# Performance work log

Hardware: AMD Instinct MI355X
Metric: run time of the kernel (lower is better)

Reference implementation:

```python
import jax, jax.numpy as jnp
import numpy as np

B, LQ, LIM = 4, 640, 1296
D_MODEL, NHEAD, DFF, MAX_DIST = 768, 12, 3072, 100
DK = D_MODEL // NHEAD
EPS = 1e-5


def _layer_norm(x, g, b):
    mu = jnp.mean(x, axis=-1, keepdims=True)
    var = jnp.mean(jnp.square(x - mu), axis=-1, keepdims=True)
    return (x - mu) * jax.lax.rsqrt(var + EPS) * g + b


def setup_inputs() -> dict:
    key = jax.random.key(0)
    ks = jax.random.split(key, 24)
    s = 0.02
    inp = {
        "docqa": jax.random.normal(ks[0], (B, LQ, D_MODEL), jnp.float32),
        "im_tokens": jax.random.normal(ks[1], (B, LIM, D_MODEL), jnp.float32),
        "docqa_x": jax.random.randint(ks[2], (B, LQ), 0, 1000, jnp.int32),
        "docqa_y": jax.random.randint(ks[3], (B, LQ), 0, 1000, jnp.int32),
        "im_tokens_x": jax.random.randint(ks[4], (B, LIM), 0, 1000, jnp.int32),
        "im_tokens_y": jax.random.randint(ks[5], (B, LIM), 0, 1000, jnp.int32),
        # attention projection params
        "Wq": jax.random.normal(ks[6], (D_MODEL, D_MODEL), jnp.float32) * s,
        "bq": jnp.zeros((D_MODEL,), jnp.float32),
        "Wk": jax.random.normal(ks[7], (D_MODEL, D_MODEL), jnp.float32) * s,
        "bk": jnp.zeros((D_MODEL,), jnp.float32),
        "Wv": jax.random.normal(ks[8], (D_MODEL, D_MODEL), jnp.float32) * s,
        "bv": jnp.zeros((D_MODEL,), jnp.float32),
        "Wo": jax.random.normal(ks[9], (D_MODEL, D_MODEL), jnp.float32) * s,
        "bo": jnp.zeros((D_MODEL,), jnp.float32),
        # relative position bias tables: (2*max_dist+1, nhead) per axis
        "bias_x": jax.random.normal(ks[10], (2 * MAX_DIST + 1, NHEAD), jnp.float32) * s,
        "bias_y": jax.random.normal(ks[11], (2 * MAX_DIST + 1, NHEAD), jnp.float32) * s,
        # FFN
        "W1": jax.random.normal(ks[12], (D_MODEL, DFF), jnp.float32) * s,
        "b1": jnp.zeros((DFF,), jnp.float32),
        "W2": jax.random.normal(ks[13], (DFF, D_MODEL), jnp.float32) * s,
        "b2": jnp.zeros((D_MODEL,), jnp.float32),
        # LayerNorms
        "g1": jnp.ones((D_MODEL,), jnp.float32),
        "be1": jnp.zeros((D_MODEL,), jnp.float32),
        "g2": jnp.ones((D_MODEL,), jnp.float32),
        "be2": jnp.zeros((D_MODEL,), jnp.float32),
    }
    return inp


def reference(docqa, im_tokens, docqa_x, docqa_y, im_tokens_x, im_tokens_y,
              Wq, bq, Wk, bk, Wv, bv, Wo, bo, bias_x, bias_y,
              W1, b1, W2, b2, g1, be1, g2, be2):
    # keys/values attend over concatenated image tokens + docqa tokens
    full = jnp.concatenate([im_tokens, docqa], axis=1)            # (B, Lk, D)
    full_x = jnp.concatenate([im_tokens_x, docqa_x], axis=1)      # (B, Lk)
    full_y = jnp.concatenate([im_tokens_y, docqa_y], axis=1)

    q = (docqa @ Wq + bq).reshape(B, LQ, NHEAD, DK)               # (B,Lq,H,Dk)
    k = (full @ Wk + bk).reshape(B, LQ + LIM, NHEAD, DK)
    v = (full @ Wv + bv).reshape(B, LQ + LIM, NHEAD, DK)

    scores = jnp.einsum("bqhd,bkhd->bhqk", q, k) / jnp.sqrt(jnp.float32(DK))

    # relative-position bias, clamped to [-max_dist, max_dist]
    rel_x = jnp.clip(docqa_x[:, :, None] - full_x[:, None, :], -MAX_DIST, MAX_DIST) + MAX_DIST
    rel_y = jnp.clip(docqa_y[:, :, None] - full_y[:, None, :], -MAX_DIST, MAX_DIST) + MAX_DIST
    pos_bias = bias_x[rel_x] + bias_y[rel_y]                      # (B,Lq,Lk,H)
    scores = scores + jnp.transpose(pos_bias, (0, 3, 1, 2))       # (B,H,Lq,Lk)

    attn = jax.nn.softmax(scores, axis=-1)
    ctx = jnp.einsum("bhqk,bkhd->bqhd", attn, v).reshape(B, LQ, D_MODEL)
    attn_out = ctx @ Wo + bo

    # residual + norm + FFN + residual + norm (dropout=0 in eval)
    src = _layer_norm(docqa + attn_out, g1, be1)
    ffn = jnp.maximum(src @ W1 + b1, 0.0) @ W2 + b2
    src = _layer_norm(src + ffn, g2, be2)
    return src
```

## Files before the change

### kernel.cpp

```cpp
#include <hip/hip_runtime.h>
#include <hip/hip_bf16.h>

constexpr int B      = 4;
constexpr int LQ     = 640;
constexpr int LIM    = 1296;
constexpr int LK     = LQ + LIM;
constexpr int DM     = 768;
constexpr int NHEAD  = 12;
constexpr int DK     = 64;
constexpr int DFF    = 3072;
constexpr int MAXD   = 100;
constexpr int M_DOC  = B * LQ;
constexpr int M_FULL = B * LK;
constexpr size_t ML_CNT = (size_t)B * NHEAD * LQ;
constexpr int NPREP  = M_FULL * (DM / 8) / 256;
constexpr int NSPLIT = 3;

typedef __attribute__((ext_vector_type(8))) short bf16x8_t;
typedef __attribute__((ext_vector_type(4))) float f32x4_t;

__device__ __forceinline__ float b2f(__hip_bfloat16 x) { return __bfloat162float(x); }

__device__ __forceinline__ float ldf(const void* p, size_t i, int f32flag) {
    return f32flag ? ((const float*)p)[i]
                   : b2f(((const __hip_bfloat16*)p)[i]);
}

__device__ __forceinline__ void gl_lds16(const void* g, void* l) {
    __builtin_amdgcn_global_load_lds(
        (const __attribute__((address_space(1))) unsigned int*)g,
        (__attribute__((address_space(3))) unsigned int*)l, 16, 0, 0);
}

__device__ __forceinline__ void wtrans_tile(const void* W, __hip_bfloat16* Wt,
                                            int f32, int K, int N, int n0, int k0,
                                            __hip_bfloat16 (*t)[33])
{
    const int tx = threadIdx.x & 31, ty = threadIdx.x >> 5;
#pragma unroll
    for (int j = 0; j < 4; ++j) {
        int k = ty + j * 8;
        t[k][tx] = __float2bfloat16(ldf(W, (size_t)(k0 + k) * N + n0 + tx, f32));
    }
    __syncthreads();
#pragma unroll
    for (int j = 0; j < 4; ++j) {
        int n = ty + j * 8;
        Wt[(size_t)(n0 + n) * K + k0 + tx] = t[tx][n];
    }
}

__global__ __launch_bounds__(256)
void prep_wt3_kernel(const void* __restrict__ g1, int* __restrict__ flagp,
                     const void* __restrict__ im, const void* __restrict__ docqa,
                     const int* __restrict__ dqx, const int* __restrict__ dqy,
                     const int* __restrict__ imx, const int* __restrict__ imy,
                     const void* __restrict__ Wq, const void* __restrict__ Wk,
                     const void* __restrict__ Wv,
                     __hip_bfloat16* __restrict__ fullA,
                     int* __restrict__ cxy,
                     __hip_bfloat16* __restrict__ Wt3)
{
    __shared__ __hip_bfloat16 t[32][33];
    const bool f32 = ((*(const unsigned*)g1) & 0xFFFFu) == 0u;
    const int bx = blockIdx.x;

    if (bx >= NPREP) {
        const int id  = bx - NPREP;
        const int wid = id / 576;
        const int tt  = id % 576;
        const void* W = (wid == 0) ? Wq : (wid == 1) ? Wk : Wv;
        wtrans_tile(W, Wt3 + (size_t)wid * DM * DM, f32 ? 1 : 0, DM, DM,
                    (tt % 24) * 32, (tt / 24) * 32, t);
        return;
    }

    if (bx == 0 && threadIdx.x == 0) *flagp = f32 ? 1 : 0;

    const int gid = bx * 256 + threadIdx.x;
    if (gid < B * LK) {
        int b = gid / LK, l = gid - b * LK;
        const int x = (l < LIM) ? imx[b * LIM + l] : dqx[b * LQ + l - LIM];
        const int y = (l < LIM) ? imy[b * LIM + l] : dqy[b * LQ + l - LIM];
        cxy[gid] = (x & 0xFFFF) | (y << 16);
    }

    const int row = gid / (DM / 8);
    const int col = (gid - row * (DM / 8)) * 8;
    const int b   = row / LK;
    const int l   = row - b * LK;
    const size_t srow = (l < LIM) ? ((size_t)(b * LIM + l)) * DM
                                  : ((size_t)(b * LQ + (l - LIM))) * DM;
    const void* src = (l < LIM) ? im : docqa;
    union { bf16x8_t v; __hip_bfloat16 h[8]; } pk;
    if (f32) {
        const float4* fp = (const float4*)((const float*)src + srow + col);
        float4 a = fp[0], c = fp[1];
        pk.h[0] = __float2bfloat16(a.x); pk.h[1] = __float2bfloat16(a.y);
        pk.h[2] = __float2bfloat16(a.z); pk.h[3] = __float2bfloat16(a.w);
        pk.h[4] = __float2bfloat16(c.x); pk.h[5] = __float2bfloat16(c.y);
        pk.h[6] = __float2bfloat16(c.z); pk.h[7] = __float2bfloat16(c.w);
    } else {
        pk.v = *(const bf16x8_t*)((const __hip_bfloat16*)src + srow + col);
    }
    *(bf16x8_t*)(fullA + (size_t)row * DM + col) = pk.v;
}

__global__ __launch_bounds__(256)
void qkv_gemm(const __hip_bfloat16* __restrict__ fullA,
              const __hip_bfloat16* __restrict__ Wt3,
              const void* __restrict__ bq,
              const void* __restrict__ bk,
              const void* __restrict__ bv,
              __hip_bfloat16* __restrict__ qout,
              __hip_bfloat16* __restrict__ kb,
              __hip_bfloat16* __restrict__ vtb,
              const int* __restrict__ flagp)
{
    __shared__ __hip_bfloat16 Als[128 * 32];
    __shared__ __hip_bfloat16 Bls[128 * 32];

    const int f32  = *flagp;
    const int tid  = threadIdx.x;
    const int lane = tid & 63;
    const int wave = tid >> 6;
    const int quad = lane >> 4;
    const int c16  = lane & 15;

    const int id = blockIdx.x;
    int n0, m0;
    if (id < 732) {
        n0 = DM + (id % 12) * 128;
        m0 = (id / 12) * 128;
    } else {
        const int t = id - 732;
        n0 = (t % 6) * 128;
        m0 = (t / 6) * 128;
    }
    const int seg = n0 / DM;

    const int wm   = (wave >> 1) * 64;
    const int wn   = (wave & 1) * 64;
    constexpr int K = DM;

    f32x4_t acc[4][4] = {};

    for (int k0 = 0; k0 < K; k0 += 32) {
#pragma unroll
        for (int p = 0; p < 2; ++p) {
            const int lin = p * 64 + lane;
            int row = wave * 32 + (lin >> 2);
            int gr  = m0 + row;
            if (seg == 0) {
                const int bb = gr / LQ;
                gr = bb * LK + LIM + (gr - bb * LQ);
            } else if (gr > M_FULL - 1) gr = M_FULL - 1;
            gl_lds16(fullA + (size_t)gr * K + k0 + (lin & 3) * 8,
                     Als + wave * 1024 + p * 512);
        }
#pragma unroll
        for (int p = 0; p < 2; ++p) {
            const int lin = p * 64 + lane;
            const int row = wave * 32 + (lin >> 2);
            gl_lds16(Wt3 + (size_t)(n0 + row) * K + k0 + (lin & 3) * 8,
                     Bls + wave * 1024 + p * 512);
        }
        __syncthreads();

        bf16x8_t af[4], bfr[4];
#pragma unroll
        for (int i = 0; i < 4; ++i)
            af[i] = *(const bf16x8_t*)(Als + (wm + i * 16 + c16) * 32 + quad * 8);
#pragma unroll
        for (int j = 0; j < 4; ++j)
            bfr[j] = *(const bf16x8_t*)(Bls + (wn + j * 16 + c16) * 32 + quad * 8);
#pragma unroll
        for (int i = 0; i < 4; ++i)
#pragma unroll
            for (int j = 0; j < 4; ++j)
                acc[i][j] = __builtin_amdgcn_mfma_f32_16x16x32_bf16(af[i], bfr[j], acc[i][j], 0, 0, 0);
        __syncthreads();
    }

    const void* bptr = (seg == 0) ? bq : (seg == 1) ? bk : bv;
#pragma unroll
    for (int j = 0; j < 4; ++j) {
        const int col  = n0 + wn + j * 16 + c16;
        const int ncol = col - seg * DM;
        const float bj = ldf(bptr, ncol, f32);
        if (seg == 2) {
            const int h = ncol >> 6, d = ncol & 63;
#pragma unroll
            for (int i = 0; i < 4; ++i) {
                const int rowb = m0 + wm + i * 16 + quad * 4;
                const int bb0  = rowb / LK;
                const int l0   = rowb - bb0 * LK;
                if (l0 + 3 < LK && rowb + 3 < M_FULL) {
                    union { ushort4 u4; __hip_bfloat16 hh[4]; } pk;
#pragma unroll
                    for (int r = 0; r < 4; ++r)
                        pk.hh[r] = __float2bfloat16(acc[i][j][r] + bj);
                    *(ushort4*)(vtb + ((size_t)((bb0 * NHEAD + h) * DK + d)) * LK + l0) = pk.u4;
                } else {
#pragma unroll
                    for (int r = 0; r < 4; ++r) {
                        const int row = rowb + r;
                        if (row < M_FULL) {
                            int bb = row / LK, l = row - bb * LK;
                            vtb[((size_t)((bb * NHEAD + h) * DK + d)) * LK + l] =
                                __float2bfloat16(acc[i][j][r] + bj);
                        }
                    }
                }
            }
        } else if (seg == 1) {
#pragma unroll
            for (int i = 0; i < 4; ++i) {
                const int rowb = m0 + wm + i * 16 + quad * 4;
#pragma unroll
                for (int r = 0; r < 4; ++r) {
                    const int row = rowb + r;
                    if (row < M_FULL)
                        kb[(size_t)row * DM + ncol] = __float2bfloat16(acc[i][j][r] + bj);
                }
            }
        } else {
#pragma unroll
            for (int i = 0; i < 4; ++i) {
                const int rowb = m0 + wm + i * 16 + quad * 4;
#pragma unroll
                for (int r = 0; r < 4; ++r)
                    qout[(size_t)(rowb + r) * DM + ncol] =
                        __float2bfloat16((acc[i][j][r] + bj) * 0.125f);
            }
        }
    }
}

__global__ __launch_bounds__(256)
void mfma_gemm_relu(const __hip_bfloat16* __restrict__ Abf,
                    const __hip_bfloat16* __restrict__ Wt,
                    const void* __restrict__ bias,
                    __hip_bfloat16* __restrict__ Cc,
                    const int* __restrict__ flagp,
                    int M, int N, int K)
{
    __shared__ __hip_bfloat16 Als[128 * 32];
    __shared__ __hip_bfloat16 Bls[128 * 32];

    const int f32  = *flagp;
    const int tid  = threadIdx.x;
    const int lane = tid & 63;
    const int wave = tid >> 6;
    const int quad = lane >> 4;
    const int c16  = lane & 15;
    const int n0   = blockIdx.x * 128;
    const int m0   = blockIdx.y * 128;
    const int wm   = (wave >> 1) * 64;
    const int wn   = (wave & 1) * 64;

    f32x4_t acc[4][4] = {};

    for (int k0 = 0; k0 < K; k0 += 32) {
#pragma unroll
        for (int p = 0; p < 2; ++p) {
            const int lin = p * 64 + lane;
            int row = wave * 32 + (lin >> 2);
            int gr  = m0 + row; if (gr > M - 1) gr = M - 1;
            gl_lds16(Abf + (size_t)gr * K + k0 + (lin & 3) * 8, Als + wave * 1024 + p * 512);
        }
#pragma unroll
        for (int p = 0; p < 2; ++p) {
            const int lin = p * 64 + lane;
            const int row = wave * 32 + (lin >> 2);
            gl_lds16(Wt + (size_t)(n0 + row) * K + k0 + (lin & 3) * 8,
                     Bls + wave * 1024 + p * 512);
        }
        __syncthreads();

        bf16x8_t af[4], bfr[4];
#pragma unroll
        for (int i = 0; i < 4; ++i)
            af[i] = *(const bf16x8_t*)(Als + (wm + i * 16 + c16) * 32 + quad * 8);
#pragma unroll
        for (int j = 0; j < 4; ++j)
            bfr[j] = *(const bf16x8_t*)(Bls + (wn + j * 16 + c16) * 32 + quad * 8);
#pragma unroll
        for (int i = 0; i < 4; ++i)
#pragma unroll
            for (int j = 0; j < 4; ++j)
                acc[i][j] = __builtin_amdgcn_mfma_f32_16x16x32_bf16(af[i], bfr[j], acc[i][j], 0, 0, 0);
        __syncthreads();
    }

#pragma unroll
    for (int j = 0; j < 4; ++j) {
        const int col = n0 + wn + j * 16 + c16;
        const float bj = ldf(bias, col, f32);
#pragma unroll
        for (int i = 0; i < 4; ++i) {
            const int rowb = m0 + wm + i * 16 + quad * 4;
#pragma unroll
            for (int r = 0; r < 4; ++r) {
                const int row = rowb + r;
                if (row < M) {
                    float v = fmaxf(acc[i][j][r] + bj, 0.f);
                    Cc[(size_t)row * N + col] = __float2bfloat16(v);
                }
            }
        }
    }
}

__global__ __launch_bounds__(256)
void sk_gemm(const __hip_bfloat16* __restrict__ Abf,
             const __hip_bfloat16* __restrict__ Wt,
             float* __restrict__ Cc,
             int M, int N, int K, int S)
{
    __shared__ __hip_bfloat16 Als[128 * 32];
    __shared__ __hip_bfloat16 Bls[128 * 32];

    const int tid  = threadIdx.x;
    const int lane = tid & 63;
    const int wave = tid >> 6;
    const int quad = lane >> 4;
    const int c16  = lane & 15;
    const int n0   = blockIdx.x * 128;
    const int m0   = blockIdx.y * 128;
    const int wm   = (wave >> 1) * 64;
    const int wn   = (wave & 1) * 64;
    const int kchunk = K / S;
    const int kbeg = blockIdx.z * kchunk;

    f32x4_t acc[4][4] = {};

    for (int k0 = kbeg; k0 < kbeg + kchunk; k0 += 32) {
#pragma unroll
        for (int p = 0; p < 2; ++p) {
            const int lin = p * 64 + lane;
            int row = wave * 32 + (lin >> 2);
            int gr  = m0 + row; if (gr > M - 1) gr = M - 1;
            gl_lds16(Abf + (size_t)gr * K + k0 + (lin & 3) * 8, Als + wave * 1024 + p * 512);
        }
#pragma unroll
        for (int p = 0; p < 2; ++p) {
            const int lin = p * 64 + lane;
            const int row = wave * 32 + (lin >> 2);
            gl_lds16(Wt + (size_t)(n0 + row) * K + k0 + (lin & 3) * 8,
                     Bls + wave * 1024 + p * 512);
        }
        __syncthreads();

        bf16x8_t af[4], bfr[4];
#pragma unroll
        for (int i = 0; i < 4; ++i)
            af[i] = *(const bf16x8_t*)(Als + (wm + i * 16 + c16) * 32 + quad * 8);
#pragma unroll
        for (int j = 0; j < 4; ++j)
            bfr[j] = *(const bf16x8_t*)(Bls + (wn + j * 16 + c16) * 32 + quad * 8);
#pragma unroll
        for (int i = 0; i < 4; ++i)
#pragma unroll
            for (int j = 0; j < 4; ++j)
                acc[i][j] = __builtin_amdgcn_mfma_f32_16x16x32_bf16(af[i], bfr[j], acc[i][j], 0, 0, 0);
        __syncthreads();
    }

#pragma unroll
    for (int j = 0; j < 4; ++j) {
        const int col = n0 + wn + j * 16 + c16;
#pragma unroll
        for (int i = 0; i < 4; ++i) {
            const int rowb = m0 + wm + i * 16 + quad * 4;
#pragma unroll
            for (int r = 0; r < 4; ++r) {
                const int row = rowb + r;
                if (row < M) atomicAdd(&Cc[(size_t)row * N + col], acc[i][j][r]);
            }
        }
    }
}

__global__ __launch_bounds__(256)
void attn_part_kernel(const __hip_bfloat16* __restrict__ Qb,
                      const __hip_bfloat16* __restrict__ Kb,
                      const __hip_bfloat16* __restrict__ Vtb,
                      const int* __restrict__ cxy,
                      const void* __restrict__ bias_x,
                      const void* __restrict__ bias_y,
                      __hip_bfloat16* __restrict__ pparts,
                      float* __restrict__ mlbase,
                      const int* __restrict__ flagp)
{
    constexpr int QT = 64, KT = 64;
    constexpr int QROW = 72;
    __shared__ char PQraw[QT * QROW * 2];
    __shared__ __hip_bfloat16 Ks[2 * KT * DK];
    __shared__ __hip_bfloat16 Vs[2 * DK * KT];
    __shared__ __hip_bfloat16 bxs[2 * MAXD + 1], bys[2 * MAXD + 1];
    __hip_bfloat16* Qs = (__hip_bfloat16*)PQraw;
    __hip_bfloat16* Ps = (__hip_bfloat16*)PQraw;

    const int f32  = *flagp;
    const int tid  = threadIdx.x;
    const int lane = tid & 63;
    const int wave = tid >> 6;
    const int quad = lane >> 4;
    const int c16  = lane & 15;

    const int id   = blockIdx.x;
    const int bh   = id % 48;
    const int rest = id / 48;
    const int s    = rest % NSPLIT;
    const int q0   = (rest / NSPLIT) * QT;
    const int b    = bh / NHEAD;
    const int h    = bh - b * NHEAD;
    const int kbeg = s * 640;
    const int kend = (s == NSPLIT - 1) ? LK : kbeg + 640;

    __hip_bfloat16* Op = pparts + (size_t)s * M_DOC * DM;
    float* mp = mlbase + (size_t)s * 2 * ML_CNT;
    float* lp = mp + ML_CNT;

    for (int i = tid; i < 2 * MAXD + 1; i += 256) {
        bxs[i] = __float2bfloat16(ldf(bias_x, (size_t)i * NHEAD + h, f32));
        bys[i] = __float2bfloat16(ldf(bias_y, (size_t)i * NHEAD + h, f32));
    }

    const __hip_bfloat16* kbase = Kb + ((size_t)(b * LK)) * DM + h * DK;
    const __hip_bfloat16* vbase = Vtb + ((size_t)((b * NHEAD + h) * DK)) * LK;
    const __hip_bfloat16* qbase = Qb + ((size_t)(b * LQ + q0)) * DM + h * DK;
    const int* cb_ = cxy + b * LK;

    const int rsub = lane >> 3;
    const int cgl  = (lane & 7) ^ (rsub & 7);

#pragma unroll
    for (int p = 0; p < 2; ++p) {
        const int rl = wave * 16 + p * 8 + rsub;
        gl_lds16(qbase + (size_t)rl * DM + cgl * 8, Qs + (wave * 16 + p * 8) * DK);
    }

#pragma unroll
    for (int p = 0; p < 2; ++p) {
        const int rl = wave * 16 + p * 8 + rsub;
        int gr = kbeg + rl; if (gr > LK - 1) gr = LK - 1;
        gl_lds16(kbase + (size_t)gr * DM + cgl * 8, Ks + (wave * 16 + p * 8) * DK);
    }
#pragma unroll
    for (int p = 0; p < 2; ++p) {
        const int dl = wave * 16 + p * 8 + rsub;
        int kks = kbeg + cgl * 8; if (kks > LK - 8) kks = LK - 8;
        gl_lds16(vbase + (size_t)dl * LK + kks, Vs + (wave * 16 + p * 8) * KT);
    }

    int qxp[4], qyp[4];
#pragma unroll
    for (int r = 0; r < 4; ++r) {
        const int v = cb_[LIM + q0 + wave * 16 + quad * 4 + r];
        qxp[r] = (v & 0xFFFF) + MAXD;
        qyp[r] = (v >> 16) + MAXD;
    }

    __syncthreads();

    const int sw  = c16 & 7;
    const int cA0 = (quad ^ sw) * 8;
    const int cA1 = ((quad + 4) ^ sw) * 8;
    const int rQ  = wave * 16 + c16;
    const bf16x8_t aq0 = *(const bf16x8_t*)(Qs + rQ * DK + cA0);
    const bf16x8_t aq1 = *(const bf16x8_t*)(Qs + rQ * DK + cA1);
    asm volatile("s_waitcnt lgkmcnt(0)" ::: "memory");
    __syncthreads();

    f32x4_t O[4] = {};
    float m_r[4], l_r[4];
#pragma unroll
    for (int r = 0; r < 4; ++r) { m_r[r] = -1e30f; l_r[r] = 0.f; }

    const int nt = (kend - kbeg + KT - 1) / KT;
    int bi = 0;
    for (int t = 0; t < nt; ++t) {
        const int k0 = kbeg + t * KT;
        {
            const int kn = k0 + KT;
            __hip_bfloat16* Kd = Ks + (bi ^ 1) * (KT * DK);
            __hip_bfloat16* Vd = Vs + (bi ^ 1) * (KT * DK);
#pragma unroll
            for (int p = 0; p < 2; ++p) {
                const int rl = wave * 16 + p * 8 + rsub;
                int gr = kn + rl; if (gr > LK - 1) gr = LK - 1;
                gl_lds16(kbase + (size_t)gr * DM + cgl * 8, Kd + (wave * 16 + p * 8) * DK);
            }
#pragma unroll
            for (int p = 0; p < 2; ++p) {
                const int dl = wave * 16 + p * 8 + rsub;
                int kks = kn + cgl * 8; if (kks > LK - 8) kks = LK - 8;
                gl_lds16(vbase + (size_t)dl * LK + kks, Vd + (wave * 16 + p * 8) * KT);
            }
        }
        const __hip_bfloat16* Kc = Ks + bi * (KT * DK);
        const __hip_bfloat16* Vc = Vs + bi * (KT * DK);

        f32x4_t S[4];
#pragma unroll
        for (int jn = 0; jn < 4; ++jn) {
            const int rK = jn * 16 + c16;
            bf16x8_t bk0 = *(const bf16x8_t*)(Kc + rK * DK + cA0);
            bf16x8_t bk1 = *(const bf16x8_t*)(Kc + rK * DK + cA1);
            f32x4_t acc = {0.f, 0.f, 0.f, 0.f};
            acc = __builtin_amdgcn_mfma_f32_16x16x32_bf16(aq0, bk0, acc, 0, 0, 0);
            acc = __builtin_amdgcn_mfma_f32_16x16x32_bf16(aq1, bk1, acc, 0, 0, 0);
            S[jn] = acc;
        }
#pragma unroll
        for (int jn = 0; jn < 4; ++jn) {
            const int kg = k0 + jn * 16 + c16;
            const bool ok = kg < LK;
            const int kv = cb_[ok ? kg : LK - 1];
            const int kx = kv & 0xFFFF, ky = kv >> 16;
#pragma unroll
            for (int r = 0; r < 4; ++r) {
                int rx = min(max(qxp[r] - kx, 0), 2 * MAXD);
                int ry = min(max(qyp[r] - ky, 0), 2 * MAXD);
                float v = S[jn][r] + b2f(bxs[rx]) + b2f(bys[ry]);
                S[jn][r] = ok ? v : -1e30f;
            }
        }
        float alpha[4];
#pragma unroll
        for (int r = 0; r < 4; ++r) {
            float mx = fmaxf(fmaxf(S[0][r], S[1][r]), fmaxf(S[2][r], S[3][r]));
            mx = fmaxf(mx, __shfl_xor(mx, 1));
            mx = fmaxf(mx, __shfl_xor(mx, 2));
            mx = fmaxf(mx, __shfl_xor(mx, 4));
            mx = fmaxf(mx, __shfl_xor(mx, 8));
            const float mt = fmaxf(m_r[r], mx);
            const float al = __expf(m_r[r] - mt);
            float sum = 0.f;
#pragma unroll
            for (int jn = 0; jn < 4; ++jn) {
                float p = __expf(S[jn][r] - mt);
                S[jn][r] = p;
                sum += p;
            }
            m_r[r] = mt;
            l_r[r] = l_r[r] * al + sum;
            alpha[r] = al;
        }
#pragma unroll
        for (int jn = 0; jn < 4; ++jn)
#pragma unroll
            for (int r = 0; r < 4; ++r)
                Ps[(wave * 16 + quad * 4 + r) * QROW + jn * 16 + c16] = __float2bfloat16(S[jn][r]);
#pragma unroll
        for (int jd = 0; jd < 4; ++jd)
#pragma unroll
            for (int r = 0; r < 4; ++r) O[jd][r] *= alpha[r];
        bf16x8_t ap0 = *(const bf16x8_t*)(Ps + (wave * 16 + c16) * QROW + quad * 8);
        bf16x8_t ap1 = *(const bf16x8_t*)(Ps + (wave * 16 + c16) * QROW + 32 + quad * 8);
#pragma unroll
        for (int jd = 0; jd < 4; ++jd) {
            const int rV = jd * 16 + c16;
            bf16x8_t bv0 = *(const bf16x8_t*)(Vc + rV * KT + cA0);
            bf16x8_t bv1 = *(const bf16x8_t*)(Vc + rV * KT + cA1);
            O[jd] = __builtin_amdgcn_mfma_f32_16x16x32_bf16(ap0, bv0, O[jd], 0, 0, 0);
            O[jd] = __builtin_amdgcn_mfma_f32_16x16x32_bf16(ap1, bv1, O[jd], 0, 0, 0);
        }
        __syncthreads();
        bi ^= 1;
    }

#pragma unroll
    for (int r = 0; r < 4; ++r) {
        float ls = l_r[r];
        ls += __shfl_xor(ls, 1);
        ls += __shfl_xor(ls, 2);
        ls += __shfl_xor(ls, 4);
        ls += __shfl_xor(ls, 8);
        const int ql = wave * 16 + quad * 4 + r;
        const size_t grow = (size_t)(b * LQ + q0 + ql);
#pragma unroll
        for (int jd = 0; jd < 4; ++jd)
            Op[grow * DM + h * DK + jd * 16 + c16] = __float2bfloat16(O[jd][r]);
        if (c16 == 0) {
            size_t mli = ((size_t)b * NHEAD + h) * LQ + q0 + ql;
            mp[mli] = m_r[r];
            lp[mli] = ls;
        }
    }
}

__global__ __launch_bounds__(256)
void merge_wt_kernel(const __hip_bfloat16* __restrict__ pparts,
                     const float* __restrict__ mlbase,
                     __hip_bfloat16* __restrict__ ctx,
                     float* __restrict__ aof,
                     const void* __restrict__ Wo,
                     __hip_bfloat16* __restrict__ WtO,
                     const void* __restrict__ W1,
                     const void* __restrict__ W2,
                     __hip_bfloat16* __restrict__ W1t,
                     __hip_bfloat16* __restrict__ W2t,
                     const int* __restrict__ flagp)
{
    __shared__ __hip_bfloat16 t[32][33];
    const int bx = blockIdx.x;

    if (bx >= M_DOC + 576) {
        const int id = bx - (M_DOC + 576);
        const int f32 = *flagp;
        const bool second = id >= 2304;
        const void* W = second ? W2 : W1;
        __hip_bfloat16* dst = second ? W2t : W1t;
        const int K = second ? DFF : DM;
        const int N = second ? DM : DFF;
        const int tt = second ? id - 2304 : id;
        const int nt = N / 32;
        wtrans_tile(W, dst, f32, K, N, (tt % nt) * 32, (tt / nt) * 32, t);
        return;
    }
    if (bx >= M_DOC) {
        const int tt = bx - M_DOC;
        wtrans_tile(Wo, WtO, *flagp, DM, DM, (tt % 24) * 32, (tt / 24) * 32, t);
        return;
    }

    const int row = bx;
    const int b = row / LQ, q = row - b * LQ;
    const int tid = threadIdx.x;
#pragma unroll
    for (int i = 0; i < 3; ++i) {
        const int c = tid + i * 256;
        const int h = c >> 6;
        const size_t mli = ((size_t)b * NHEAD + h) * LQ + q;
        const float m0 = mlbase[mli],                  l0 = mlbase[ML_CNT + mli];
        const float m1 = mlbase[2 * ML_CNT + mli],     l1 = mlbase[3 * ML_CNT + mli];
        const float m2 = mlbase[4 * ML_CNT + mli],     l2 = mlbase[5 * ML_CNT + mli];
        const float mm = fmaxf(m0, fmaxf(m1, m2));
        const float w0 = __expf(m0 - mm), w1 = __expf(m1 - mm), w2 = __expf(m2 - mm);
        const float denom = l0 * w0 + l1 * w1 + l2 * w2;
        const size_t idx = (size_t)row * DM + c;
        const float v = (b2f(pparts[idx]) * w0 +
                         b2f(pparts[(size_t)M_DOC * DM + idx]) * w1 +
                         b2f(pparts[(size_t)2 * M_DOC * DM + idx]) * w2) / denom;
        ctx[idx] = __float2bfloat16(v);
        aof[idx] = 0.f;
    }
}

template<int MODE>
__global__ __launch_bounds__(256)
void ln_kernel(const void* __restrict__ Xin,
               const __hip_bfloat16* __restrict__ Xb,
               const float* __restrict__ Xf2f,
               const void* __restrict__ bias2,
               const void* __restrict__ g,
               const void* __restrict__ be,
               __hip_bfloat16* __restrict__ outb,
               void* __restrict__ outv,
               float* __restrict__ zbuf,
               const int* __restrict__ flagp)
{
    __shared__ float red1[4], red2[4];
    const int f32 = *flagp;
    const int row = blockIdx.x;
    const int tid = threadIdx.x;
    const int lane = tid & 63;
    const int wave = tid >> 6;

    float x[3];
#pragma unroll
    for (int i = 0; i < 3; ++i) {
        int c = tid + i * 256;
        size_t idx = (size_t)row * DM + c;
        float a  = (MODE == 0) ? ldf(Xin, idx, f32) : b2f(Xb[idx]);
        x[i] = a + Xf2f[idx] + ldf(bias2, c, f32);
    }
    float s1 = x[0] + x[1] + x[2];
    float s2 = x[0] * x[0] + x[1] * x[1] + x[2] * x[2];
#pragma unroll
    for (int off = 32; off > 0; off >>= 1) {
        s1 += __shfl_xor(s1, off);
        s2 += __shfl_xor(s2, off);
    }
    if (lane == 0) { red1[wave] = s1; red2[wave] = s2; }
    __syncthreads();
    s1 = red1[0] + red1[1] + red1[2] + red1[3];
    s2 = red2[0] + red2[1] + red2[2] + red2[3];
    float mu   = s1 * (1.f / DM);
    float var  = s2 * (1.f / DM) - mu * mu;
    float rstd = rsqrtf(var + 1e-5f);
#pragma unroll
    for (int i = 0; i < 3; ++i) {
        int c = tid + i * 256;
        size_t idx = (size_t)row * DM + c;
        float v = (x[i] - mu) * rstd * ldf(g, c, f32) + ldf(be, c, f32);
        if (MODE == 0) {
            outb[idx] = __float2bfloat16(v);
            zbuf[idx] = 0.f;
        } else {
            if (f32) ((float*)outv)[idx] = v;
            else     ((__hip_bfloat16*)outv)[idx] = __float2bfloat16(v);
        }
    }
}

extern "C" void kernel_launch(void* const* d_in, const int* in_sizes, int n_in,
                              void* d_out, int out_size, void* d_ws, size_t ws_size,
                              hipStream_t stream)
{
    const void* docqa = d_in[0];
    const void* im    = d_in[1];
    const int* dqx = (const int*)d_in[2];
    const int* dqy = (const int*)d_in[3];
    const int* imx = (const int*)d_in[4];
    const int* imy = (const int*)d_in[5];
    const void* Wq = d_in[6];
    const void* bq = d_in[7];
    const void* Wk = d_in[8];
    const void* bk = d_in[9];
    const void* Wv = d_in[10];
    const void* bv = d_in[11];
    const void* Wo = d_in[12];
    const void* bo = d_in[13];
    const void* bias_x = d_in[14];
    const void* bias_y = d_in[15];
    const void* W1 = d_in[16];
    const void* b1 = d_in[17];
    const void* W2 = d_in[18];
    const void* b2 = d_in[19];
    const void* g1  = d_in[20];
    const void* be1 = d_in[21];
    const void* g2  = d_in[22];
    const void* be2 = d_in[23];

    char* w = (char*)d_ws;
    int*            flagp = (int*)w;
    __hip_bfloat16* qR  = (__hip_bfloat16*)(w + 256);
    __hip_bfloat16* kb  = qR + (size_t)M_DOC  * DM;
    __hip_bfloat16* vtb = kb + (size_t)M_FULL * DM;
    __hip_bfloat16* cb  = vtb + (size_t)M_FULL * DM;
    char* cbB = (char*)cb;
    char* r1B = (char*)qR;

    __hip_bfloat16* fullA = cb;
    __hip_bfloat16* Wt3  = qR;
    int*            cxyp = (int*)(r1B + 3538944);
    __hip_bfloat16* WtO  = qR;
    __hip_bfloat16* qout = (__hip_bfloat16*)d_out;
    __hip_bfloat16* pparts = cb;
    float*          mlb  = (float*)(r1B + 1179648);
    __hip_bfloat16* ctx  = cb;
    __hip_bfloat16* src1 = cb;
    float*          fof  = (float*)(cbB + 3932160);
    float*          aof  = (float*)kb;
    __hip_bfloat16* W1t  = vtb;
    __hip_bfloat16* W2t  = vtb + (size_t)DFF * DM;
    __hip_bfloat16* mid  = qR;

    dim3 blk(256);

    prep_wt3_kernel<<<dim3(NPREP + 3 * 576), blk, 0, stream>>>(
        g1, flagp, im, docqa, dqx, dqy, imx, imy, Wq, Wk, Wv, fullA, cxyp, Wt3);
    qkv_gemm<<<dim3(732 + 120), blk, 0, stream>>>(
        fullA, Wt3, bq, bk, bv, qout, kb, vtb, flagp);
    attn_part_kernel<<<dim3(48 * 30), blk, 0, stream>>>(
        qout, kb, vtb, cxyp, bias_x, bias_y, pparts, mlb, flagp);
    merge_wt_kernel<<<dim3(M_DOC + 576 + 4608), blk, 0, stream>>>(
        pparts, mlb, ctx, aof, Wo, WtO, W1, W2, W1t, W2t, flagp);
    sk_gemm<<<dim3(DM / 128, M_DOC / 128, 4), blk, 0, stream>>>(
        ctx, WtO, aof, M_DOC, DM, DM, 4);
    ln_kernel<0><<<dim3(M_DOC), blk, 0, stream>>>(
        docqa, nullptr, aof, bo, g1, be1, src1, nullptr, fof, flagp);
    mfma_gemm_relu<<<dim3(DFF / 128, M_DOC / 128), blk, 0, stream>>>(
        src1, W1t, b1, mid, flagp, M_DOC, DFF, DM);
    sk_gemm<<<dim3(DM / 128, M_DOC / 128, 4), blk, 0, stream>>>(
        mid, W2t, fof, M_DOC, DM, DFF, 4);
    ln_kernel<1><<<dim3(M_DOC), blk, 0, stream>>>(
        nullptr, src1, fof, b2, g2, be2, nullptr, d_out, nullptr, flagp);
}
```

Before: 378.1 us.

## Double-buffer LDS tiles in QKV, FFN and split-K GEMM kernels

Each GEMM main loop now uses two LDS buffers for the A and B tiles. It issues the global-to-LDS load for the next k-tile before running MFMAs on the current one, and drops one barrier per iteration. The aim is to overlap global memory latency with matrix-core work. In exchange, LDS use per block doubles, which may lower occupancy, and the final iteration issues a redundant reload of the last tile.

```diff
diff --git a/kernel.cpp b/kernel.cpp
--- a/kernel.cpp
+++ b/kernel.cpp
@@ -117,8 +117,8 @@
               __hip_bfloat16* __restrict__ vtb,
               const int* __restrict__ flagp)
 {
-    __shared__ __hip_bfloat16 Als[128 * 32];
-    __shared__ __hip_bfloat16 Bls[128 * 32];
+    __shared__ __hip_bfloat16 Als[2 * 128 * 32];
+    __shared__ __hip_bfloat16 Bls[2 * 128 * 32];
 
     const int f32  = *flagp;
     const int tid  = threadIdx.x;
@@ -143,9 +143,7 @@
     const int wn   = (wave & 1) * 64;
     constexpr int K = DM;
 
-    f32x4_t acc[4][4] = {};
-
-    for (int k0 = 0; k0 < K; k0 += 32) {
+    auto stage = [&](int kk, int buf) {
 #pragma unroll
         for (int p = 0; p < 2; ++p) {
             const int lin = p * 64 + lane;
@@ -155,31 +153,44 @@
                 const int bb = gr / LQ;
                 gr = bb * LK + LIM + (gr - bb * LQ);
             } else if (gr > M_FULL - 1) gr = M_FULL - 1;
-            gl_lds16(fullA + (size_t)gr * K + k0 + (lin & 3) * 8,
-                     Als + wave * 1024 + p * 512);
+            gl_lds16(fullA + (size_t)gr * K + kk + (lin & 3) * 8,
+                     Als + buf * 4096 + wave * 1024 + p * 512);
         }
 #pragma unroll
         for (int p = 0; p < 2; ++p) {
             const int lin = p * 64 + lane;
             const int row = wave * 32 + (lin >> 2);
-            gl_lds16(Wt3 + (size_t)(n0 + row) * K + k0 + (lin & 3) * 8,
-                     Bls + wave * 1024 + p * 512);
-        }
-        __syncthreads();
-
+            gl_lds16(Wt3 + (size_t)(n0 + row) * K + kk + (lin & 3) * 8,
+                     Bls + buf * 4096 + wave * 1024 + p * 512);
+        }
+    };
+
+    f32x4_t acc[4][4] = {};
+
+    stage(0, 0);
+    __syncthreads();
+    int bi = 0;
+    for (int t = 0; t < K / 32; ++t) {
+        const int k0 = t * 32;
+        const int kn = (k0 + 32 > K - 32) ? (K - 32) : (k0 + 32);
+        stage(kn, bi ^ 1);
+
+        const __hip_bfloat16* Ac = Als + bi * 4096;
+        const __hip_bfloat16* Bc = Bls + bi * 4096;
         bf16x8_t af[4], bfr[4];
 #pragma unroll
         for (int i = 0; i < 4; ++i)
-            af[i] = *(const bf16x8_t*)(Als + (wm + i * 16 + c16) * 32 + quad * 8);
+            af[i] = *(const bf16x8_t*)(Ac + (wm + i * 16 + c16) * 32 + quad * 8);
 #pragma unroll
         for (int j = 0; j < 4; ++j)
-            bfr[j] = *(const bf16x8_t*)(Bls + (wn + j * 16 + c16) * 32 + quad * 8);
+            bfr[j] = *(const bf16x8_t*)(Bc + (wn + j * 16 + c16) * 32 + quad * 8);
 #pragma unroll
         for (int i = 0; i < 4; ++i)
 #pragma unroll
             for (int j = 0; j < 4; ++j)
                 acc[i][j] = __builtin_amdgcn_mfma_f32_16x16x32_bf16(af[i], bfr[j], acc[i][j], 0, 0, 0);
         __syncthreads();
+        bi ^= 1;
     }
 
     const void* bptr = (seg == 0) ? bq : (seg == 1) ? bk : bv;
@@ -245,8 +256,8 @@
                     const int* __restrict__ flagp,
                     int M, int N, int K)
 {
-    __shared__ __hip_bfloat16 Als[128 * 32];
-    __shared__ __hip_bfloat16 Bls[128 * 32];
+    __shared__ __hip_bfloat16 Als[2 * 128 * 32];
+    __shared__ __hip_bfloat16 Bls[2 * 128 * 32];
 
     const int f32  = *flagp;
     const int tid  = threadIdx.x;
@@ -259,38 +270,51 @@
     const int wm   = (wave >> 1) * 64;
     const int wn   = (wave & 1) * 64;
 
-    f32x4_t acc[4][4] = {};
-
-    for (int k0 = 0; k0 < K; k0 += 32) {
+    auto stage = [&](int kk, int buf) {
 #pragma unroll
         for (int p = 0; p < 2; ++p) {
             const int lin = p * 64 + lane;
             int row = wave * 32 + (lin >> 2);
             int gr  = m0 + row; if (gr > M - 1) gr = M - 1;
-            gl_lds16(Abf + (size_t)gr * K + k0 + (lin & 3) * 8, Als + wave * 1024 + p * 512);
+            gl_lds16(Abf + (size_t)gr * K + kk + (lin & 3) * 8,
+                     Als + buf * 4096 + wave * 1024 + p * 512);
         }
 #pragma unroll
         for (int p = 0; p < 2; ++p) {
             const int lin = p * 64 + lane;
             const int row = wave * 32 + (lin >> 2);
-            gl_lds16(Wt + (size_t)(n0 + row) * K + k0 + (lin & 3) * 8,
-                     Bls + wave * 1024 + p * 512);
-        }
-        __syncthreads();
-
+            gl_lds16(Wt + (size_t)(n0 + row) * K + kk + (lin & 3) * 8,
+                     Bls + buf * 4096 + wave * 1024 + p * 512);
+        }
+    };
+
+    f32x4_t acc[4][4] = {};
+
+    stage(0, 0);
+    __syncthreads();
+    int bi = 0;
+    const int nt = K / 32;
+    for (int t = 0; t < nt; ++t) {
+        const int k0 = t * 32;
+        const int kn = (k0 + 32 > K - 32) ? (K - 32) : (k0 + 32);
+        stage(kn, bi ^ 1);
+
+        const __hip_bfloat16* Ac = Als + bi * 4096;
+        const __hip_bfloat16* Bc = Bls + bi * 4096;
         bf16x8_t af[4], bfr[4];
 #pragma unroll
         for (int i = 0; i < 4; ++i)
-            af[i] = *(const bf16x8_t*)(Als + (wm + i * 16 + c16) * 32 + quad * 8);
+            af[i] = *(const bf16x8_t*)(Ac + (wm + i * 16 + c16) * 32 + quad * 8);
 #pragma unroll
         for (int j = 0; j < 4; ++j)
-            bfr[j] = *(const bf16x8_t*)(Bls + (wn + j * 16 + c16) * 32 + quad * 8);
+            bfr[j] = *(const bf16x8_t*)(Bc + (wn + j * 16 + c16) * 32 + quad * 8);
 #pragma unroll
         for (int i = 0; i < 4; ++i)
 #pragma unroll
             for (int j = 0; j < 4; ++j)
                 acc[i][j] = __builtin_amdgcn_mfma_f32_16x16x32_bf16(af[i], bfr[j], acc[i][j], 0, 0, 0);
         __syncthreads();
+        bi ^= 1;
     }
 
 #pragma unroll
@@ -318,8 +342,8 @@
              float* __restrict__ Cc,
              int M, int N, int K, int S)
 {
-    __shared__ __hip_bfloat16 Als[128 * 32];
-    __shared__ __hip_bfloat16 Bls[128 * 32];
+    __shared__ __hip_bfloat16 Als[2 * 128 * 32];
+    __shared__ __hip_bfloat16 Bls[2 * 128 * 32];
 
     const int tid  = threadIdx.x;
     const int lane = tid & 63;
@@ -332,39 +356,53 @@
     const int wn   = (wave & 1) * 64;
     const int kchunk = K / S;
     const int kbeg = blockIdx.z * kchunk;
-
-    f32x4_t acc[4][4] = {};
-
-    for (int k0 = kbeg; k0 < kbeg + kchunk; k0 += 32) {
+    const int klast = kbeg + kchunk - 32;
+
+    auto stage = [&](int kk, int buf) {
 #pragma unroll
         for (int p = 0; p < 2; ++p) {
             const int lin = p * 64 + lane;
             int row = wave * 32 + (lin >> 2);
             int gr  = m0 + row; if (gr > M - 1) gr = M - 1;
-            gl_lds16(Abf + (size_t)gr * K + k0 + (lin & 3) * 8, Als + wave * 1024 + p * 512);
+            gl_lds16(Abf + (size_t)gr * K + kk + (lin & 3) * 8,
+                     Als + buf * 4096 + wave * 1024 + p * 512);
         }
 #pragma unroll
         for (int p = 0; p < 2; ++p) {
             const int lin = p * 64 + lane;
             const int row = wave * 32 + (lin >> 2);
-            gl_lds16(Wt + (size_t)(n0 + row) * K + k0 + (lin & 3) * 8,
-                     Bls + wave * 1024 + p * 512);
-        }
-        __syncthreads();
-
+            gl_lds16(Wt + (size_t)(n0 + row) * K + kk + (lin & 3) * 8,
+                     Bls + buf * 4096 + wave * 1024 + p * 512);
+        }
+    };
+
+    f32x4_t acc[4][4] = {};
+
+    stage(kbeg, 0);
+    __syncthreads();
+    int bi = 0;
+    const int nt = kchunk / 32;
+    for (int t = 0; t < nt; ++t) {
+        const int k0 = kbeg + t * 32;
+        const int kn = (k0 + 32 > klast) ? klast : (k0 + 32);
+        stage(kn, bi ^ 1);
+
+        const __hip_bfloat16* Ac = Als + bi * 4096;
+        const __hip_bfloat16* Bc = Bls + bi * 4096;
         bf16x8_t af[4], bfr[4];
 #pragma unroll
         for (int i = 0; i < 4; ++i)
-            af[i] = *(const bf16x8_t*)(Als + (wm + i * 16 + c16) * 32 + quad * 8);
+            af[i] = *(const bf16x8_t*)(Ac + (wm + i * 16 + c16) * 32 + quad * 8);
 #pragma unroll
         for (int j = 0; j < 4; ++j)
-            bfr[j] = *(const bf16x8_t*)(Bls + (wn + j * 16 + c16) * 32 + quad * 8);
+            bfr[j] = *(const bf16x8_t*)(Bc + (wn + j * 16 + c16) * 32 + quad * 8);
 #pragma unroll
         for (int i = 0; i < 4; ++i)
 #pragma unroll
             for (int j = 0; j < 4; ++j)
                 acc[i][j] = __builtin_amdgcn_mfma_f32_16x16x32_bf16(af[i], bfr[j], acc[i][j], 0, 0, 0);
         __syncthreads();
+        bi ^= 1;
     }
 
 #pragma unroll
```

Result: slower. 386.0 us (+2.1%).
